# Kernel optimization log

Hardware: AMD Instinct MI355X
Metric: run time of the kernel (lower is better)

Reference implementation:

```python
import jax, jax.numpy as jnp
import numpy as np

B_SZ, S, D = 8, 512, 768
H = 12                 # num_heads
N_EXP = 8              # num_experts
RANK = 16
ALPHA = 32
TOP_K = 2


def setup_inputs() -> dict:
    key = jax.random.key(0)
    ks = jax.random.split(key, 9)
    x = jax.random.normal(ks[0], (B_SZ, S, D), jnp.float32)
    W_qkv = jax.random.normal(ks[1], (3 * D, D), jnp.float32) * 0.02
    b_qkv = jnp.zeros((3 * D,), jnp.float32)
    W_gate = jax.random.normal(ks[2], (N_EXP, D), jnp.float32) * 0.02
    b_gate = jnp.zeros((N_EXP,), jnp.float32)
    A = jax.random.normal(ks[3], (N_EXP, RANK, D), jnp.float32) * 0.02      # LoRA down
    B_lora = jax.random.normal(ks[4], (N_EXP, 3 * D, RANK), jnp.float32) * 0.02  # LoRA up
    W_proj = jax.random.normal(ks[5], (D, D), jnp.float32) * 0.02
    b_proj = jnp.zeros((D,), jnp.float32)
    return {"x": x, "W_qkv": W_qkv, "b_qkv": b_qkv, "W_gate": W_gate,
            "b_gate": b_gate, "A": A, "B_lora": B_lora,
            "W_proj": W_proj, "b_proj": b_proj}


def reference(x, W_qkv, b_qkv, W_gate, b_gate, A, B_lora, W_proj, b_proj):
    b, s, d = x.shape
    n_exp, rank = A.shape[0], A.shape[1]
    scaling = ALPHA / rank
    head_dim = d // H
    scale = head_dim ** -0.5
    t = b * s
    x_flat = x.reshape(t, d)                                   # [T, D]

    # frozen qkv base projection
    qkv_base = x @ W_qkv.T + b_qkv                             # [B, S, 3D]

    # router: softmax gating + top-k
    logits = x_flat @ W_gate.T + b_gate                        # [T, N]
    router_probs = jax.nn.softmax(logits, axis=-1)
    top_k_weights, top_k_indices = jax.lax.top_k(router_probs, TOP_K)  # [T, k]

    # batched LoRA: compute-all-experts
    a_down = jnp.einsum('td,nrd->tnr', x_flat, A)              # [T, N, r]
    expert_out = jnp.einsum('tnr,nor->tno', a_down, B_lora) * scaling  # [T, N, 3D]

    # dispatch tensor: scatter top-k weights into [T, N]
    dispatch = jnp.zeros((t, n_exp), x.dtype).at[
        jnp.arange(t)[:, None], top_k_indices].add(top_k_weights)
    sparse_out = jnp.einsum('tno,tn->to', expert_out, dispatch)  # [T, 3D]

    qkv = (qkv_base + sparse_out.reshape(b, s, 3 * d))
    qkv = qkv.reshape(b, s, 3, H, head_dim).transpose(2, 0, 3, 1, 4)  # [3, B, H, S, hd]
    q, k, v = qkv[0], qkv[1], qkv[2]

    attn = jax.nn.softmax(jnp.einsum('bhqd,bhkd->bhqk', q, k) * scale, axis=-1)
    out = jnp.einsum('bhqk,bhkd->bhqd', attn, v)
    out = out.transpose(0, 2, 1, 3).reshape(b, s, d)
    return out @ W_proj.T + b_proj
```

## Files before the change

kernel.cpp:

```cpp
#include <hip/hip_runtime.h>
#include <hip/hip_bf16.h>

#define B_SZ 8
#define SEQ 512
#define D 768
#define D3 2304
#define NH 12
#define HD 64
#define NE 8
#define RANK 16
#define TT (B_SZ * SEQ)
#define SCALING 2.0f
#define KE 2304
#define KQ 2560
#define EK 192
#define NBH (B_SZ * NH)

typedef __attribute__((ext_vector_type(8))) short bh8;
typedef __attribute__((ext_vector_type(4))) float fx4;

__device__ __forceinline__ unsigned short f2bf_rne(float x) {
    unsigned u = __float_as_uint(x);
    unsigned r = (u + 0x7FFFu + ((u >> 16) & 1u)) >> 16;
    return (unsigned short)r;
}
__device__ __forceinline__ float bf2f(unsigned short b) {
    return __uint_as_float(((unsigned)b) << 16);
}
__device__ __forceinline__ void load_lds16(const void* g, void* l) {
    __builtin_amdgcn_global_load_lds(
        (const __attribute__((address_space(1))) unsigned int*)g,
        (__attribute__((address_space(3))) unsigned int*)l,
        16, 0, 0);
}

template <int RS, bool ALAY>
__global__ __launch_bounds__(256) void k_convert(
    const float* __restrict__ in, unsigned short* __restrict__ out, int M)
{
    const int gid = blockIdx.x * 256 + threadIdx.x;
    if (gid >= M * 192) return;
    const int r = gid / 192;
    const int c4 = gid - r * 192;
    const float4 v = ((const float4*)(in + (size_t)r * D))[c4];
    ushort4 hi, lo;
    hi.x = f2bf_rne(v.x); hi.y = f2bf_rne(v.y);
    hi.z = f2bf_rne(v.z); hi.w = f2bf_rne(v.w);
    lo.x = f2bf_rne(v.x - bf2f(hi.x)); lo.y = f2bf_rne(v.y - bf2f(hi.y));
    lo.z = f2bf_rne(v.z - bf2f(hi.z)); lo.w = f2bf_rne(v.w - bf2f(hi.w));
    ushort4* row = (ushort4*)(out + (size_t)r * RS);
    row[c4] = hi;
    row[c4 + 192] = ALAY ? hi : lo;
    row[c4 + 384] = ALAY ? lo : hi;
}

__global__ __launch_bounds__(256) void k_blora(
    const float* __restrict__ Bup, unsigned short* __restrict__ B2)
{
    const int gid = blockIdx.x * 256 + threadIdx.x;
    if (gid >= D3 * 128) return;
    const int n = gid >> 7;
    const int p = gid & 127;
    const int e = p >> 4, r = p & 15;
    const unsigned short h = f2bf_rne(Bup[((size_t)e * D3 + n) * RANK + r]);
    B2[(size_t)n * KQ + 2304 + p] = h;
    B2[(size_t)n * KQ + 2432 + p] = h;
}

__global__ __launch_bounds__(64) void k_router(
    const float* __restrict__ x, const float* __restrict__ Wg,
    const float* __restrict__ bg, const float* __restrict__ A,
    unsigned short* __restrict__ A2)
{
    const int t = blockIdx.x;
    const int l = threadIdx.x;
    const float* xr = x + (size_t)t * D;

    float xv[12];
#pragma unroll
    for (int i = 0; i < 12; ++i) xv[i] = xr[l + 64 * i];

    float p[NE];
#pragma unroll
    for (int e = 0; e < NE; ++e) {
        const float* w = Wg + (size_t)e * D;
        float s = 0.f;
#pragma unroll
        for (int i = 0; i < 12; ++i) s += xv[i] * w[l + 64 * i];
#pragma unroll
        for (int off = 32; off; off >>= 1) s += __shfl_xor(s, off);
        p[e] = s + bg[e];
    }
    float mx = p[0];
#pragma unroll
    for (int e = 1; e < NE; ++e) mx = fmaxf(mx, p[e]);
    float den = 0.f;
#pragma unroll
    for (int e = 0; e < NE; ++e) { p[e] = expf(p[e] - mx); den += p[e]; }
    int i0 = 0;
#pragma unroll
    for (int e = 1; e < NE; ++e) if (p[e] > p[i0]) i0 = e;
    int i1 = (i0 == 0) ? 1 : 0;
#pragma unroll
    for (int e = 0; e < NE; ++e) if (e != i1 && e != i0 && p[e] > p[i1]) i1 = e;
    const float w0 = p[i0] / den * SCALING;
    const float w1 = p[i1] / den * SCALING;

    unsigned short tv0 = 0, tv1 = 0, tv2 = 0, tv3 = 0;
    const int base = 4 * l;

#pragma unroll
    for (int j = 0; j < 2; ++j) {
        const int e = j ? i1 : i0;
        const float wj = j ? w1 : w0;
        const float* Ae = A + (size_t)e * RANK * D;
#pragma unroll
        for (int r = 0; r < RANK; ++r) {
            const float* a = Ae + (size_t)r * D;
            float s = 0.f;
#pragma unroll
            for (int i = 0; i < 12; ++i) s += xv[i] * a[l + 64 * i];
#pragma unroll
            for (int off = 32; off; off >>= 1) s += __shfl_xor(s, off);
            const float val = s * wj;
            const unsigned short hi = f2bf_rne(val);
            const unsigned short lo = f2bf_rne(val - bf2f(hi));
            const int ph = e * 16 + r;
            const int pl = ph + 128;
            tv0 = (base + 0 == ph) ? hi : ((base + 0 == pl) ? lo : tv0);
            tv1 = (base + 1 == ph) ? hi : ((base + 1 == pl) ? lo : tv1);
            tv2 = (base + 2 == ph) ? hi : ((base + 2 == pl) ? lo : tv2);
            tv3 = (base + 3 == ph) ? hi : ((base + 3 == pl) ? lo : tv3);
        }
    }
    ushort4 tq; tq.x = tv0; tq.y = tv1; tq.z = tv2; tq.w = tv3;
    *(ushort4*)(A2 + (size_t)t * KQ + 2304 + base) = tq;
}

template <int FM, int FN, int EPI>
__global__ __launch_bounds__(256) void k_gemm_mfma(
    const unsigned short* __restrict__ Ae, const unsigned short* __restrict__ Be,
    const float* __restrict__ bias, float* __restrict__ C,
    int N, int K2,
    unsigned short* __restrict__ Qe, unsigned short* __restrict__ Ke,
    unsigned short* __restrict__ Vt)
{
    constexpr int BM = 2 * FM * 16;
    constexpr int BN = 2 * FN * 16;
    constexpr int ISS_A = BM / 32;
    constexpr int ISS_B = BN / 32;
    __shared__ __align__(16) unsigned short As[BM * 64];
    __shared__ __align__(16) unsigned short Bs[BN * 64];

    const int id = blockIdx.y * gridDim.x + blockIdx.x;
    const int cpx = (gridDim.x * gridDim.y) >> 3;
    const int swz = (id & 7) * cpx + (id >> 3);
    const int gx = swz % gridDim.x;
    const int gy = swz / gridDim.x;

    const int tid = threadIdx.x;
    const int lane = tid & 63;
    const int wv = tid >> 6;
    const int wr = wv >> 1, wc = wv & 1;
    const int m0 = gy * BM;
    const int n0 = gx * BN;

    fx4 acc[FM][FN] = {};

    const int arow = wv * 8 + (lane >> 3);
    const int acol = (((lane & 7) ^ (lane >> 3)) << 3);
    const int frow = lane & 15;

    for (int k0 = 0; k0 < K2; k0 += 64) {
#pragma unroll
        for (int i = 0; i < ISS_A; ++i)
            load_lds16(Ae + (size_t)(m0 + i * 32 + arow) * K2 + k0 + acol,
                       (char*)As + i * 4096 + wv * 1024);
#pragma unroll
        for (int i = 0; i < ISS_B; ++i)
            load_lds16(Be + (size_t)(n0 + i * 32 + arow) * K2 + k0 + acol,
                       (char*)Bs + i * 4096 + wv * 1024);
        __syncthreads();
#pragma unroll
        for (int kk = 0; kk < 2; ++kk) {
            const int un = ((((kk << 2) | (lane >> 4)) ^ (lane & 7)) << 3);
            bh8 afr[FM], bfr[FN];
#pragma unroll
            for (int i = 0; i < FM; ++i)
                afr[i] = *(const bh8*)&As[(wr * FM * 16 + i * 16 + frow) * 64 + un];
#pragma unroll
            for (int j = 0; j < FN; ++j)
                bfr[j] = *(const bh8*)&Bs[(wc * FN * 16 + j * 16 + frow) * 64 + un];
#pragma unroll
            for (int i = 0; i < FM; ++i)
#pragma unroll
                for (int j = 0; j < FN; ++j)
                    acc[i][j] = __builtin_amdgcn_mfma_f32_16x16x32_bf16(
                        afr[i], bfr[j], acc[i][j], 0, 0, 0);
        }
        __syncthreads();
    }

    const int col = lane & 15;
    const int rbase = (lane >> 4) * 4;

    if (EPI == 0) {
#pragma unroll
        for (int i = 0; i < FM; ++i) {
#pragma unroll
            for (int r = 0; r < 4; ++r) {
                const int m = m0 + wr * FM * 16 + i * 16 + rbase + r;
#pragma unroll
                for (int j = 0; j < FN; ++j) {
                    const int n = n0 + wc * FN * 16 + j * 16 + col;
                    C[(size_t)m * N + n] = acc[i][j][r] + bias[n];
                }
            }
        }
    } else {
        const int sec = n0 / D;
#pragma unroll
        for (int i = 0; i < FM; ++i) {
            const int mb = m0 + wr * FM * 16 + i * 16 + rbase;
#pragma unroll
            for (int j = 0; j < FN; ++j) {
                const int n = n0 + wc * FN * 16 + j * 16 + col;
                const int n2 = n - sec * D;
                const int h = n2 >> 6, d0 = n2 & 63;
                const float bi = bias[n];
                if (sec == 2) {
                    ushort4 vq;
                    vq.x = f2bf_rne(acc[i][j][0] + bi);
                    vq.y = f2bf_rne(acc[i][j][1] + bi);
                    vq.z = f2bf_rne(acc[i][j][2] + bi);
                    vq.w = f2bf_rne(acc[i][j][3] + bi);
                    const int b = mb >> 9, s = mb & 511;
                    *(ushort4*)(Vt + ((size_t)(b * NH + h) * HD + d0) * SEQ + s) = vq;
                } else {
#pragma unroll
                    for (int r = 0; r < 4; ++r) {
                        const int m = mb + r;
                        const int b = m >> 9, s = m & 511;
                        float c = acc[i][j][r] + bi;
                        if (sec == 0) c *= 0.125f;
                        const unsigned short hi = f2bf_rne(c);
                        const unsigned short lo = f2bf_rne(c - bf2f(hi));
                        unsigned short* row =
                            (sec == 0 ? Qe : Ke) + ((size_t)(b * NH + h) * SEQ + s) * EK;
                        if (sec == 0) {
                            row[d0] = hi; row[64 + d0] = hi; row[128 + d0] = lo;
                        } else {
                            row[d0] = hi; row[64 + d0] = lo; row[128 + d0] = hi;
                        }
                    }
                }
            }
        }
    }
}

__global__ __launch_bounds__(256) void k_attn_mfma(
    const unsigned short* __restrict__ Qe, const unsigned short* __restrict__ Ke,
    const unsigned short* __restrict__ Vt, unsigned short* __restrict__ Ae2)
{
    __shared__ __align__(16) unsigned short Ks[64 * 200];
    __shared__ __align__(16) unsigned short Vs[64 * 72];
    __shared__ __align__(16) unsigned short Ps[4 * 16 * 72];

    const int bid = blockIdx.x;
    const int qb = bid & 7;
    const int bh = bid >> 3;
    const int b = bh / NH, h = bh - b * NH;
    const int tid = threadIdx.x;
    const int lane = tid & 63;
    const int wv = tid >> 6;
    const int lg = lane >> 4;
    const int lr = lane & 15;
    const int q0 = qb * 64 + wv * 16;

    bh8 qa[6];
    {
        const unsigned short* qrow = Qe + ((size_t)bh * SEQ + q0 + lr) * EK + lg * 8;
#pragma unroll
        for (int kc = 0; kc < 6; ++kc)
            qa[kc] = *(const bh8*)(qrow + kc * 32);
    }

    fx4 o[4] = {};
    float m4[4], l4[4];
#pragma unroll
    for (int r = 0; r < 4; ++r) { m4[r] = -INFINITY; l4[r] = 0.f; }

    const int sr = tid >> 2, sc = tid & 3;
    bh8 kreg[6], vreg[2];
    {
        const unsigned short* ksrc = Ke + ((size_t)bh * SEQ + sr) * EK + sc * 48;
#pragma unroll
        for (int j = 0; j < 6; ++j) kreg[j] = *(const bh8*)(ksrc + j * 8);
        const unsigned short* vsrc = Vt + ((size_t)bh * HD + sr) * SEQ + sc * 16;
#pragma unroll
        for (int j = 0; j < 2; ++j) vreg[j] = *(const bh8*)(vsrc + j * 8);
    }

    for (int kt = 0; kt < 8; ++kt) {
        __syncthreads();
#pragma unroll
        for (int j = 0; j < 6; ++j)
            *(bh8*)&Ks[sr * 200 + sc * 48 + j * 8] = kreg[j];
#pragma unroll
        for (int j = 0; j < 2; ++j)
            *(bh8*)&Vs[sr * 72 + sc * 16 + j * 8] = vreg[j];
        __syncthreads();
        if (kt < 7) {
            const int kv1 = (kt + 1) * 64;
            const unsigned short* ksrc = Ke + ((size_t)bh * SEQ + kv1 + sr) * EK + sc * 48;
#pragma unroll
            for (int j = 0; j < 6; ++j) kreg[j] = *(const bh8*)(ksrc + j * 8);
            const unsigned short* vsrc = Vt + ((size_t)bh * HD + sr) * SEQ + kv1 + sc * 16;
#pragma unroll
            for (int j = 0; j < 2; ++j) vreg[j] = *(const bh8*)(vsrc + j * 8);
        }

        fx4 sf[4] = {};
        __builtin_amdgcn_s_setprio(1);
#pragma unroll
        for (int kc = 0; kc < 6; ++kc) {
            bh8 kb[4];
#pragma unroll
            for (int j = 0; j < 4; ++j)
                kb[j] = *(const bh8*)&Ks[(j * 16 + lr) * 200 + kc * 32 + lg * 8];
#pragma unroll
            for (int j = 0; j < 4; ++j)
                sf[j] = __builtin_amdgcn_mfma_f32_16x16x32_bf16(qa[kc], kb[j], sf[j], 0, 0, 0);
        }
        __builtin_amdgcn_s_setprio(0);

        float mxr[4];
#pragma unroll
        for (int r = 0; r < 4; ++r)
            mxr[r] = fmaxf(fmaxf(sf[0][r], sf[1][r]), fmaxf(sf[2][r], sf[3][r]));
#pragma unroll
        for (int off = 1; off < 16; off <<= 1)
#pragma unroll
            for (int r = 0; r < 4; ++r)
                mxr[r] = fmaxf(mxr[r], __shfl_xor(mxr[r], off));
        float corr[4];
#pragma unroll
        for (int r = 0; r < 4; ++r) {
            const float mn = fmaxf(m4[r], mxr[r]);
            corr[r] = expf(m4[r] - mn);
            m4[r] = mn;
        }
#pragma unroll
        for (int j = 0; j < 4; ++j)
#pragma unroll
            for (int r = 0; r < 4; ++r)
                sf[j][r] = expf(sf[j][r] - m4[r]);
        float rs[4];
#pragma unroll
        for (int r = 0; r < 4; ++r)
            rs[r] = (sf[0][r] + sf[1][r]) + (sf[2][r] + sf[3][r]);
#pragma unroll
        for (int off = 1; off < 16; off <<= 1)
#pragma unroll
            for (int r = 0; r < 4; ++r)
                rs[r] += __shfl_xor(rs[r], off);
#pragma unroll
        for (int r = 0; r < 4; ++r)
            l4[r] = l4[r] * corr[r] + rs[r];
#pragma unroll
        for (int j = 0; j < 4; ++j)
#pragma unroll
            for (int r = 0; r < 4; ++r)
                o[j][r] *= corr[r];

        unsigned short* pw = Ps + wv * (16 * 72);
#pragma unroll
        for (int j = 0; j < 4; ++j)
#pragma unroll
            for (int r = 0; r < 4; ++r)
                pw[(lg * 4 + r) * 72 + j * 16 + lr] = f2bf_rne(sf[j][r]);

        __builtin_amdgcn_s_setprio(1);
#pragma unroll
        for (int kc = 0; kc < 2; ++kc) {
            bh8 pa = *(const bh8*)&pw[lr * 72 + kc * 32 + lg * 8];
            bh8 vb[4];
#pragma unroll
            for (int j = 0; j < 4; ++j)
                vb[j] = *(const bh8*)&Vs[(j * 16 + lr) * 72 + kc * 32 + lg * 8];
#pragma unroll
            for (int j = 0; j < 4; ++j)
                o[j] = __builtin_amdgcn_mfma_f32_16x16x32_bf16(pa, vb[j], o[j], 0, 0, 0);
        }
        __builtin_amdgcn_s_setprio(0);
    }

    float inv[4];
#pragma unroll
    for (int r = 0; r < 4; ++r) inv[r] = 1.f / l4[r];
    const int trow = b * SEQ + q0 + lg * 4;
#pragma unroll
    for (int r = 0; r < 4; ++r) {
        unsigned short* row = Ae2 + (size_t)(trow + r) * KE;
#pragma unroll
        for (int j = 0; j < 4; ++j) {
            const float v = o[j][r] * inv[r];
            const unsigned short hi = f2bf_rne(v);
            const unsigned short lo = f2bf_rne(v - bf2f(hi));
            const int c = h * HD + j * 16 + lr;
            row[c] = hi; row[768 + c] = hi; row[1536 + c] = lo;
        }
    }
}

extern "C" void kernel_launch(void* const* d_in, const int* in_sizes, int n_in,
                              void* d_out, int out_size, void* d_ws, size_t ws_size,
                              hipStream_t stream)
{
    const float* x      = (const float*)d_in[0];
    const float* W_qkv  = (const float*)d_in[1];
    const float* b_qkv  = (const float*)d_in[2];
    const float* W_gate = (const float*)d_in[3];
    const float* b_gate = (const float*)d_in[4];
    const float* A      = (const float*)d_in[5];
    const float* B_lora = (const float*)d_in[6];
    const float* W_proj = (const float*)d_in[7];
    const float* b_proj = (const float*)d_in[8];
    float* out = (float*)d_out;

    unsigned short* A2  = (unsigned short*)d_ws;
    unsigned short* B2  = A2 + (size_t)TT * KQ;
    unsigned short* Qe  = B2 + (size_t)D3 * KQ;
    unsigned short* Ke  = Qe + (size_t)NBH * SEQ * EK;
    unsigned short* Vt  = Ke + (size_t)NBH * SEQ * EK;
    unsigned short* Wpe = Vt + (size_t)NBH * HD * SEQ;
    unsigned short* Ae2 = A2;

    k_convert<KQ, true ><<<(TT * 192 + 255) / 256, 256, 0, stream>>>(x, A2, TT);
    k_convert<KQ, false><<<(D3 * 192 + 255) / 256, 256, 0, stream>>>(W_qkv, B2, D3);
    k_blora<<<(D3 * 128 + 255) / 256, 256, 0, stream>>>(B_lora, B2);
    k_router<<<TT, 64, 0, stream>>>(x, W_gate, b_gate, A, A2);
    k_convert<KE, false><<<(D * 192 + 255) / 256, 256, 0, stream>>>(W_proj, Wpe, D);

    {
        dim3 grid(D3 / 96, TT / 128);
        k_gemm_mfma<4, 3, 1><<<grid, 256, 0, stream>>>(
            A2, B2, b_qkv, nullptr, D3, KQ, Qe, Ke, Vt);
    }

    k_attn_mfma<<<NBH * 8, 256, 0, stream>>>(Qe, Ke, Vt, Ae2);

    {
        dim3 grid(D / 96, TT / 64);
        k_gemm_mfma<2, 3, 0><<<grid, 256, 0, stream>>>(
            Ae2, Wpe, b_proj, out, D, KE, nullptr, nullptr, nullptr);
    }
}
```

Baseline: 173.5 us.

## Merge prep kernels into one launch; store Q/K as fp32 and split in attention

Five preprocessing launches (input/weight bf16 hi-lo conversion, LoRA-B packing, router) become a single kernel that dispatches on block index, removing launch gaps. The QKV GEMM epilogue now writes Q and K as plain fp32 instead of triple-width bf16 hi/lo layouts. The attention kernel performs the hi/lo split itself when loading Q and each K tile. This cuts the scattered 2-byte epilogue stores and the intermediate bytes written, at the cost of extra conversion ALU work inside attention.

```diff
diff --git a/kernel.cpp b/kernel.cpp
--- a/kernel.cpp
+++ b/kernel.cpp
@@ -13,7 +13,6 @@
 #define SCALING 2.0f
 #define KE 2304
 #define KQ 2560
-#define EK 192
 #define NBH (B_SZ * NH)
 
 typedef __attribute__((ext_vector_type(8))) short bh8;
@@ -33,13 +32,19 @@
         (__attribute__((address_space(3))) unsigned int*)l,
         16, 0, 0);
 }
+template <int BASE>
+__device__ __forceinline__ void split4(float4 v, bh8& hi, bh8& lo) {
+    unsigned short h;
+    h = f2bf_rne(v.x); hi[BASE+0]=(short)h; lo[BASE+0]=(short)f2bf_rne(v.x - bf2f(h));
+    h = f2bf_rne(v.y); hi[BASE+1]=(short)h; lo[BASE+1]=(short)f2bf_rne(v.y - bf2f(h));
+    h = f2bf_rne(v.z); hi[BASE+2]=(short)h; lo[BASE+2]=(short)f2bf_rne(v.z - bf2f(h));
+    h = f2bf_rne(v.w); hi[BASE+3]=(short)h; lo[BASE+3]=(short)f2bf_rne(v.w - bf2f(h));
+}
 
 template <int RS, bool ALAY>
-__global__ __launch_bounds__(256) void k_convert(
-    const float* __restrict__ in, unsigned short* __restrict__ out, int M)
-{
-    const int gid = blockIdx.x * 256 + threadIdx.x;
-    if (gid >= M * 192) return;
+__device__ __forceinline__ void conv_body(
+    const float* __restrict__ in, unsigned short* __restrict__ out, int gid)
+{
     const int r = gid / 192;
     const int c4 = gid - r * 192;
     const float4 v = ((const float4*)(in + (size_t)r * D))[c4];
@@ -54,28 +59,12 @@
     row[c4 + 384] = ALAY ? lo : hi;
 }
 
-__global__ __launch_bounds__(256) void k_blora(
-    const float* __restrict__ Bup, unsigned short* __restrict__ B2)
-{
-    const int gid = blockIdx.x * 256 + threadIdx.x;
-    if (gid >= D3 * 128) return;
-    const int n = gid >> 7;
-    const int p = gid & 127;
-    const int e = p >> 4, r = p & 15;
-    const unsigned short h = f2bf_rne(Bup[((size_t)e * D3 + n) * RANK + r]);
-    B2[(size_t)n * KQ + 2304 + p] = h;
-    B2[(size_t)n * KQ + 2432 + p] = h;
-}
-
-__global__ __launch_bounds__(64) void k_router(
+__device__ __forceinline__ void router_body(
     const float* __restrict__ x, const float* __restrict__ Wg,
     const float* __restrict__ bg, const float* __restrict__ A,
-    unsigned short* __restrict__ A2)
-{
-    const int t = blockIdx.x;
-    const int l = threadIdx.x;
+    unsigned short* __restrict__ A2, int t, int l)
+{
     const float* xr = x + (size_t)t * D;
-
     float xv[12];
 #pragma unroll
     for (int i = 0; i < 12; ++i) xv[i] = xr[l + 64 * i];
@@ -108,7 +97,6 @@
 
     unsigned short tv0 = 0, tv1 = 0, tv2 = 0, tv3 = 0;
     const int base = 4 * l;
-
 #pragma unroll
     for (int j = 0; j < 2; ++j) {
         const int e = j ? i1 : i0;
@@ -137,12 +125,41 @@
     *(ushort4*)(A2 + (size_t)t * KQ + 2304 + base) = tq;
 }
 
+__global__ __launch_bounds__(256) void k_prep(
+    const float* __restrict__ x, const float* __restrict__ Wq,
+    const float* __restrict__ Wp, const float* __restrict__ Bup,
+    const float* __restrict__ Wg, const float* __restrict__ bg,
+    const float* __restrict__ A,
+    unsigned short* __restrict__ A2, unsigned short* __restrict__ B2,
+    unsigned short* __restrict__ Wpe)
+{
+    const int bid = blockIdx.x;
+    const int tid = threadIdx.x;
+    if (bid < 3072) {
+        conv_body<KQ, true >(x, A2, bid * 256 + tid);
+    } else if (bid < 4800) {
+        conv_body<KQ, false>(Wq, B2, (bid - 3072) * 256 + tid);
+    } else if (bid < 5952) {
+        const int gid = (bid - 4800) * 256 + tid;
+        const int n = gid >> 7;
+        const int p = gid & 127;
+        const int e = p >> 4, r = p & 15;
+        const unsigned short h = f2bf_rne(Bup[((size_t)e * D3 + n) * RANK + r]);
+        B2[(size_t)n * KQ + 2304 + p] = h;
+        B2[(size_t)n * KQ + 2432 + p] = h;
+    } else if (bid < 6528) {
+        conv_body<KE, false>(Wp, Wpe, (bid - 5952) * 256 + tid);
+    } else {
+        router_body(x, Wg, bg, A, A2, (bid - 6528) * 4 + (tid >> 6), tid & 63);
+    }
+}
+
 template <int FM, int FN, int EPI>
 __global__ __launch_bounds__(256) void k_gemm_mfma(
     const unsigned short* __restrict__ Ae, const unsigned short* __restrict__ Be,
     const float* __restrict__ bias, float* __restrict__ C,
     int N, int K2,
-    unsigned short* __restrict__ Qe, unsigned short* __restrict__ Ke,
+    float* __restrict__ Qf, float* __restrict__ Kf,
     unsigned short* __restrict__ Vt)
 {
     constexpr int BM = 2 * FM * 16;
@@ -237,21 +254,14 @@
                     const int b = mb >> 9, s = mb & 511;
                     *(ushort4*)(Vt + ((size_t)(b * NH + h) * HD + d0) * SEQ + s) = vq;
                 } else {
+                    float* dst = (sec == 0) ? Qf : Kf;
 #pragma unroll
                     for (int r = 0; r < 4; ++r) {
                         const int m = mb + r;
                         const int b = m >> 9, s = m & 511;
                         float c = acc[i][j][r] + bi;
                         if (sec == 0) c *= 0.125f;
-                        const unsigned short hi = f2bf_rne(c);
-                        const unsigned short lo = f2bf_rne(c - bf2f(hi));
-                        unsigned short* row =
-                            (sec == 0 ? Qe : Ke) + ((size_t)(b * NH + h) * SEQ + s) * EK;
-                        if (sec == 0) {
-                            row[d0] = hi; row[64 + d0] = hi; row[128 + d0] = lo;
-                        } else {
-                            row[d0] = hi; row[64 + d0] = lo; row[128 + d0] = hi;
-                        }
+                        dst[((size_t)(b * NH + h) * SEQ + s) * HD + d0] = c;
                     }
                 }
             }
@@ -260,7 +270,7 @@
 }
 
 __global__ __launch_bounds__(256) void k_attn_mfma(
-    const unsigned short* __restrict__ Qe, const unsigned short* __restrict__ Ke,
+    const float* __restrict__ Qf, const float* __restrict__ Kf,
     const unsigned short* __restrict__ Vt, unsigned short* __restrict__ Ae2)
 {
     __shared__ __align__(16) unsigned short Ks[64 * 200];
@@ -278,13 +288,17 @@
     const int lr = lane & 15;
     const int q0 = qb * 64 + wv * 16;
 
-    bh8 qa[6];
+    bh8 qh0, qh1, ql0, ql1;
     {
-        const unsigned short* qrow = Qe + ((size_t)bh * SEQ + q0 + lr) * EK + lg * 8;
-#pragma unroll
-        for (int kc = 0; kc < 6; ++kc)
-            qa[kc] = *(const bh8*)(qrow + kc * 32);
-    }
+        const float* qrow = Qf + ((size_t)bh * SEQ + q0 + lr) * HD + lg * 8;
+        float4 a0 = ((const float4*)qrow)[0];
+        float4 a1 = ((const float4*)qrow)[1];
+        float4 b0 = ((const float4*)(qrow + 32))[0];
+        float4 b1 = ((const float4*)(qrow + 32))[1];
+        split4<0>(a0, qh0, ql0); split4<4>(a1, qh0, ql0);
+        split4<0>(b0, qh1, ql1); split4<4>(b1, qh1, ql1);
+    }
+    bh8 qa[6] = {qh0, qh1, qh0, qh1, ql0, ql1};
 
     fx4 o[4] = {};
     float m4[4], l4[4];
@@ -292,30 +306,37 @@
     for (int r = 0; r < 4; ++r) { m4[r] = -INFINITY; l4[r] = 0.f; }
 
     const int sr = tid >> 2, sc = tid & 3;
-    bh8 kreg[6], vreg[2];
+    float4 kf0, kf1, kf2, kf3;
+    bh8 vreg[2];
     {
-        const unsigned short* ksrc = Ke + ((size_t)bh * SEQ + sr) * EK + sc * 48;
-#pragma unroll
-        for (int j = 0; j < 6; ++j) kreg[j] = *(const bh8*)(ksrc + j * 8);
+        const float* ksrc = Kf + ((size_t)bh * SEQ + sr) * HD + sc * 16;
+        kf0 = ((const float4*)ksrc)[0]; kf1 = ((const float4*)ksrc)[1];
+        kf2 = ((const float4*)ksrc)[2]; kf3 = ((const float4*)ksrc)[3];
         const unsigned short* vsrc = Vt + ((size_t)bh * HD + sr) * SEQ + sc * 16;
 #pragma unroll
         for (int j = 0; j < 2; ++j) vreg[j] = *(const bh8*)(vsrc + j * 8);
     }
 
     for (int kt = 0; kt < 8; ++kt) {
+        bh8 kh0, kh1, kl0, kl1;
+        split4<0>(kf0, kh0, kl0); split4<4>(kf1, kh0, kl0);
+        split4<0>(kf2, kh1, kl1); split4<4>(kf3, kh1, kl1);
         __syncthreads();
-#pragma unroll
-        for (int j = 0; j < 6; ++j)
-            *(bh8*)&Ks[sr * 200 + sc * 48 + j * 8] = kreg[j];
+        {
+            unsigned short* krow = &Ks[sr * 200 + sc * 16];
+            *(bh8*)(krow)       = kh0; *(bh8*)(krow + 8)   = kh1;
+            *(bh8*)(krow + 64)  = kl0; *(bh8*)(krow + 72)  = kl1;
+            *(bh8*)(krow + 128) = kh0; *(bh8*)(krow + 136) = kh1;
+        }
 #pragma unroll
         for (int j = 0; j < 2; ++j)
             *(bh8*)&Vs[sr * 72 + sc * 16 + j * 8] = vreg[j];
         __syncthreads();
         if (kt < 7) {
             const int kv1 = (kt + 1) * 64;
-            const unsigned short* ksrc = Ke + ((size_t)bh * SEQ + kv1 + sr) * EK + sc * 48;
-#pragma unroll
-            for (int j = 0; j < 6; ++j) kreg[j] = *(const bh8*)(ksrc + j * 8);
+            const float* ksrc = Kf + ((size_t)bh * SEQ + kv1 + sr) * HD + sc * 16;
+            kf0 = ((const float4*)ksrc)[0]; kf1 = ((const float4*)ksrc)[1];
+            kf2 = ((const float4*)ksrc)[2]; kf3 = ((const float4*)ksrc)[3];
             const unsigned short* vsrc = Vt + ((size_t)bh * HD + sr) * SEQ + kv1 + sc * 16;
 #pragma unroll
             for (int j = 0; j < 2; ++j) vreg[j] = *(const bh8*)(vsrc + j * 8);
@@ -431,25 +452,22 @@
 
     unsigned short* A2  = (unsigned short*)d_ws;
     unsigned short* B2  = A2 + (size_t)TT * KQ;
-    unsigned short* Qe  = B2 + (size_t)D3 * KQ;
-    unsigned short* Ke  = Qe + (size_t)NBH * SEQ * EK;
-    unsigned short* Vt  = Ke + (size_t)NBH * SEQ * EK;
+    float* Qf           = (float*)(B2 + (size_t)D3 * KQ);
+    float* Kf           = Qf + (size_t)NBH * SEQ * HD;
+    unsigned short* Vt  = (unsigned short*)(Kf + (size_t)NBH * SEQ * HD);
     unsigned short* Wpe = Vt + (size_t)NBH * HD * SEQ;
     unsigned short* Ae2 = A2;
 
-    k_convert<KQ, true ><<<(TT * 192 + 255) / 256, 256, 0, stream>>>(x, A2, TT);
-    k_convert<KQ, false><<<(D3 * 192 + 255) / 256, 256, 0, stream>>>(W_qkv, B2, D3);
-    k_blora<<<(D3 * 128 + 255) / 256, 256, 0, stream>>>(B_lora, B2);
-    k_router<<<TT, 64, 0, stream>>>(x, W_gate, b_gate, A, A2);
-    k_convert<KE, false><<<(D * 192 + 255) / 256, 256, 0, stream>>>(W_proj, Wpe, D);
+    k_prep<<<7552, 256, 0, stream>>>(x, W_qkv, W_proj, B_lora,
+                                     W_gate, b_gate, A, A2, B2, Wpe);
 
     {
         dim3 grid(D3 / 96, TT / 128);
         k_gemm_mfma<4, 3, 1><<<grid, 256, 0, stream>>>(
-            A2, B2, b_qkv, nullptr, D3, KQ, Qe, Ke, Vt);
-    }
-
-    k_attn_mfma<<<NBH * 8, 256, 0, stream>>>(Qe, Ke, Vt, Ae2);
+            A2, B2, b_qkv, nullptr, D3, KQ, Qf, Kf, Vt);
+    }
+
+    k_attn_mfma<<<NBH * 8, 256, 0, stream>>>(Qf, Kf, Vt, Ae2);
 
     {
         dim3 grid(D / 96, TT / 64);
```

Measured after the change: 179.1 us. +3.2%, slower.
